# Kernel tuning notes

Hardware: AMD Instinct MI355X
Metric: run time of the kernel (lower is better)

The kernel has to match this reference:

```python
import jax, jax.numpy as jnp
import numpy as np

N, B, D_IN, HID = 1024, 8, 256, 256
L, SH, LH, GH = 2, 2, 4, 2
H = SH + LH + GH
DH = HID // H
EPS = 1e-5


def _sinusoidal_pe(n, d):
    pos = np.arange(n, dtype=np.float32)[:, None]
    i = np.arange(d, dtype=np.float32)[None, :]
    angle = pos / np.power(10000.0, (2.0 * np.floor(i / 2.0)) / d)
    pe = np.where((np.arange(d) % 2) == 0, np.sin(angle), np.cos(angle))
    return jnp.asarray(pe, jnp.float32)  # (n, d)


def _ln(x, g, b):
    mu = x.mean(-1, keepdims=True)
    var = ((x - mu) ** 2).mean(-1, keepdims=True)
    return (x - mu) * jax.lax.rsqrt(var + EPS) * g + b


def setup_inputs() -> dict:
    key = jax.random.key(0)
    ks = jax.random.split(key, 16)
    s = 0.02
    inp = {
        "nodes": jax.random.normal(ks[0], (N, B, D_IN), jnp.float32),
        "dist": jax.random.randint(ks[1], (B, N, N), 0, 6, jnp.int32),
        "W_in": jax.random.normal(ks[2], (D_IN, HID), jnp.float32) * s,
        "b_in": jnp.zeros((HID,), jnp.float32),
        "ln_in_g": jnp.ones((HID,), jnp.float32),
        "ln_in_b": jnp.zeros((HID,), jnp.float32),
        "Wqkv": jax.random.normal(ks[3], (L, HID, 3 * HID), jnp.float32) * s,
        "bqkv": jnp.zeros((L, 3 * HID), jnp.float32),
        "Wo": jax.random.normal(ks[4], (L, HID, HID), jnp.float32) * s,
        "bo": jnp.zeros((L, HID), jnp.float32),
        "ln1_g": jnp.ones((L, HID), jnp.float32),
        "ln1_b": jnp.zeros((L, HID), jnp.float32),
        "W1": jax.random.normal(ks[5], (L, HID, 2 * HID), jnp.float32) * s,
        "b1": jnp.zeros((L, 2 * HID), jnp.float32),
        "W2": jax.random.normal(ks[6], (L, 2 * HID, HID), jnp.float32) * s,
        "b2": jnp.zeros((L, HID), jnp.float32),
        "ln2_g": jnp.ones((L, HID), jnp.float32),
        "ln2_b": jnp.zeros((L, HID), jnp.float32),
        "bn_g": jnp.ones((HID,), jnp.float32),
        "bn_b": jnp.zeros((HID,), jnp.float32),
    }
    return inp


def reference(nodes, dist, W_in, b_in, ln_in_g, ln_in_b, Wqkv, bqkv, Wo, bo,
              ln1_g, ln1_b, W1, b1, W2, b2, ln2_g, ln2_b, bn_g, bn_b):
    # positional embedding (sinusoidal, added) + dense + LayerNorm; dropout=eval (identity)
    x = nodes + _sinusoidal_pe(N, D_IN)[:, None, :]          # (N,B,D_IN)
    x = _ln(x @ W_in + b_in, ln_in_g, ln_in_b)               # (N,B,HID)

    # dist_to_mask: per-head-group allowed patterns; True in torch mask = disallowed
    short = (dist == 1)[:, None]                             # (B,1,N,N)
    longm = (dist >= 1)[:, None]
    allowed = jnp.concatenate([
        jnp.broadcast_to(short, (B, SH, N, N)),
        jnp.broadcast_to(longm, (B, LH, N, N)),
        jnp.ones((B, GH, N, N), bool),
    ], axis=1)                                               # (B,H,N,N)
    bias = jnp.where(allowed, 0.0, -jnp.inf).astype(x.dtype)

    scale = 1.0 / np.sqrt(DH)
    for l in range(L):
        qkv = x @ Wqkv[l] + bqkv[l]                          # (N,B,3*HID)
        q, k, v = jnp.split(qkv, 3, axis=-1)
        def heads(t):  # (N,B,HID) -> (B,H,N,DH)
            return t.reshape(N, B, H, DH).transpose(1, 2, 0, 3)
        q, k, v = heads(q), heads(k), heads(v)
        s = jnp.einsum('bhnd,bhmd->bhnm', q, k) * scale + bias
        a = jax.nn.softmax(s, axis=-1)
        o = jnp.einsum('bhnm,bhmd->bhnd', a, v)              # (B,H,N,DH)
        o = o.transpose(2, 0, 1, 3).reshape(N, B, HID)
        x = _ln(x + o @ Wo[l] + bo[l], ln1_g[l], ln1_b[l])   # post-norm
        f = jax.nn.relu(x @ W1[l] + b1[l]) @ W2[l] + b2[l]
        x = _ln(x + f, ln2_g[l], ln2_b[l])

    y = x[0]                                                 # (B,HID) first position
    mu = y.mean(0)
    var = ((y - mu) ** 2).mean(0)
    return (y - mu) * jax.lax.rsqrt(var + EPS) * bn_g + bn_b
```

## Files before the change

### kernel.cpp

```cpp
#include <hip/hip_runtime.h>
#include <math.h>

constexpr int Nn = 1024, Bb = 8, HIDc = 256, Hh = 8, DHc = 32;

typedef __bf16 bf16x8 __attribute__((ext_vector_type(8)));
typedef __bf16 bf16x4 __attribute__((ext_vector_type(4)));
typedef float  f32x4  __attribute__((ext_vector_type(4)));

struct WCvtArgs {
    const float* src[9];
    int K[9], M[9], dstOff[9], tiles[9];
};

__global__ __launch_bounds__(256)
void prep_k(WCvtArgs a, __bf16* __restrict__ Wt,
            const int* __restrict__ dist, unsigned char* __restrict__ mp,
            const float* __restrict__ nodes, __bf16* __restrict__ xinb)
{
    __shared__ float ts[32][33];
    const int tid = threadIdx.x;
    if (blockIdx.x < 1088) {
        int bid = blockIdx.x, i = 0;
        while (bid >= a.tiles[i]) { bid -= a.tiles[i]; ++i; }
        const int K = a.K[i], M = a.M[i];
        const int tilesM = M >> 5;
        const int m0 = (bid % tilesM) << 5, k0 = (bid / tilesM) << 5;
        const float* src = a.src[i];
        __bf16* dst = Wt + a.dstOff[i];
        const int tx = tid & 31, ty = tid >> 5;
        #pragma unroll
        for (int j = 0; j < 4; ++j)
            ts[ty + 8 * j][tx] = src[(size_t)(k0 + ty + 8 * j) * M + m0 + tx];
        __syncthreads();
        #pragma unroll
        for (int j = 0; j < 4; ++j)
            dst[(size_t)(m0 + ty + 8 * j) * K + k0 + tx] = (__bf16)ts[tx][ty + 8 * j];
    } else if (blockIdx.x < 3136) {
        const int idx = (blockIdx.x - 1088) * 256 + tid;
        const int quad = idx & 3, c = (idx >> 2) & 15, q = (idx >> 6) & 1023, b = idx >> 16;
        const int* dp = dist + ((((size_t)b << 10) + q) << 10) + c * 64 + quad * 4;
        uchar4 out;
        unsigned char* po = &out.x;
        #pragma unroll
        for (int t = 0; t < 4; ++t) {
            const int4 v = *(const int4*)(dp + t * 16);
            unsigned int code = 0;
            const int dd[4] = {v.x, v.y, v.z, v.w};
            #pragma unroll
            for (int r = 0; r < 4; ++r)
                code |= ((dd[r] == 1 ? 1u : 0u) | (dd[r] >= 1 ? 2u : 0u)) << (2 * r);
            po[t] = (unsigned char)code;
        }
        *(uchar4*)(mp + ((((size_t)b << 10) + q) << 8) + (c << 4) + (quad << 2)) = out;
    } else {
        const int idx = (blockIdx.x - 3136) * 256 + tid;
        const int token = idx >> 7, k2 = (idx & 127) * 2;
        const int b = token >> 10, n = token & 1023;
        const float e = (float)k2 * (1.0f / 256.0f);
        const float freq = exp2f(-13.287712379549449f * e);
        const float ang = (float)n * freq;
        const float2 nd = *(const float2*)(nodes + ((size_t)(n * 8 + b)) * 256 + k2);
        __bf16* p = xinb + (size_t)token * 256 + k2;
        p[0] = (__bf16)(nd.x + sinf(ang));
        p[1] = (__bf16)(nd.y + cosf(ang));
    }
}

template<int NCH>
__device__ __forceinline__ void gemm8(const bf16x8* af, const __bf16* __restrict__ wsrc,
                                      __bf16 (*wlds)[72], int mrow, int kcol,
                                      int ch, int col, int quad, f32x4* acc)
{
    constexpr int K = NCH * 64;
    bf16x8 wreg[8];
    #pragma unroll
    for (int i = 0; i < 8; ++i)
        wreg[i] = *(const bf16x8*)(wsrc + (size_t)(i * 32 + mrow) * K + kcol);
    #pragma unroll
    for (int t = 0; t < 8; ++t) acc[t] = (f32x4){0.f, 0.f, 0.f, 0.f};
    for (int ck = 0; ck < NCH; ++ck) {
        __syncthreads();
        #pragma unroll
        for (int i = 0; i < 8; ++i)
            *(bf16x8*)&wlds[i * 32 + mrow][kcol] = wreg[i];
        if (ck + 1 < NCH) {
            #pragma unroll
            for (int i = 0; i < 8; ++i)
                wreg[i] = *(const bf16x8*)(wsrc + (size_t)(i * 32 + mrow) * K + (ck + 1) * 64 + kcol);
        }
        __syncthreads();
        #pragma unroll
        for (int t = 0; t < 8; ++t)
            #pragma unroll
            for (int kc = 0; kc < 2; ++kc) {
                const bf16x8 bfr = *(const bf16x8*)(&wlds[ch * 128 + t * 16 + col][kc * 32 + quad * 8]);
                acc[t] = __builtin_amdgcn_mfma_f32_16x16x32_bf16(af[ck * 2 + kc], bfr, acc[t], 0, 0, 0);
            }
    }
}

template<bool RESID, bool FFN, bool QKV, bool LASTX>
__global__ __launch_bounds__(256)
void layer_k(const __bf16* __restrict__ Ain, const float* __restrict__ xres,
             const __bf16* __restrict__ w0, const float* __restrict__ b0,
             const float* __restrict__ g1, const float* __restrict__ be1,
             const __bf16* __restrict__ w1, const float* __restrict__ b1_,
             const __bf16* __restrict__ w2, const float* __restrict__ b2_,
             const float* __restrict__ g2, const float* __restrict__ be2,
             const __bf16* __restrict__ wq, const float* __restrict__ bq,
             float* __restrict__ xout,
             __bf16* __restrict__ qb, __bf16* __restrict__ kb, __bf16* __restrict__ vtb)
{
    __shared__ char smem[36864];
    __bf16 (*wlds)[72]  = (__bf16 (*)[72])smem;
    __bf16 (*trans)[520] = (__bf16 (*)[520])smem;
    __shared__ float red[2][2][16][2];

    const int tid = threadIdx.x;
    const int lane = tid & 63;
    const int wv = tid >> 6;
    const int rt = wv >> 1, ch = wv & 1;
    const int col = lane & 15, quad = lane >> 4;
    const int row0 = blockIdx.x * 32;
    const int rowL = rt * 16 + col;
    const int mrow = tid >> 3, kcol = (tid & 7) * 8;
    const int trow = rt * 16 + quad * 4;

    bf16x8 afA[8];
    #pragma unroll
    for (int kc = 0; kc < 8; ++kc)
        afA[kc] = *(const bf16x8*)(Ain + (size_t)(row0 + rowL) * 256 + kc * 32 + quad * 8);
    f32x4 acc[8];
    gemm8<4>(afA, w0, wlds, mrow, kcol, ch, col, quad, acc);

    float val[4][8];
    {
        float bb[8], gm[8], bt[8];
        #pragma unroll
        for (int t = 0; t < 8; ++t) {
            const int cc = ch * 128 + t * 16 + col;
            bb[t] = b0[cc]; gm[t] = g1[cc]; bt[t] = be1[cc];
        }
        #pragma unroll
        for (int r = 0; r < 4; ++r) {
            float s1 = 0.f, s2 = 0.f;
            #pragma unroll
            for (int t = 0; t < 8; ++t) {
                float v = acc[t][r] + bb[t];
                if (RESID) v += xres[(size_t)(row0 + trow + r) * 256 + ch * 128 + t * 16 + col];
                val[r][t] = v; s1 += v; s2 += v * v;
            }
            s1 += __shfl_xor(s1, 1); s1 += __shfl_xor(s1, 2);
            s1 += __shfl_xor(s1, 4); s1 += __shfl_xor(s1, 8);
            s2 += __shfl_xor(s2, 1); s2 += __shfl_xor(s2, 2);
            s2 += __shfl_xor(s2, 4); s2 += __shfl_xor(s2, 8);
            if (col == 0) { red[rt][ch][quad * 4 + r][0] = s1; red[rt][ch][quad * 4 + r][1] = s2; }
        }
        __syncthreads();
        #pragma unroll
        for (int r = 0; r < 4; ++r) {
            const int qr = quad * 4 + r;
            const float s1 = red[rt][0][qr][0] + red[rt][1][qr][0];
            const float s2 = red[rt][0][qr][1] + red[rt][1][qr][1];
            const float mu = s1 * (1.0f / 256.0f);
            const float rv = rsqrtf(s2 * (1.0f / 256.0f) - mu * mu + 1e-5f);
            #pragma unroll
            for (int t = 0; t < 8; ++t) {
                const float o = (val[r][t] - mu) * rv * gm[t] + bt[t];
                val[r][t] = o;
                trans[trow + r][ch * 128 + t * 16 + col] = (__bf16)o;
                if (!FFN)
                    xout[(size_t)(row0 + trow + r) * 256 + ch * 128 + t * 16 + col] = o;
            }
        }
        __syncthreads();
    }

    if (FFN) {
        bf16x8 af1[8];
        #pragma unroll
        for (int kc = 0; kc < 8; ++kc)
            af1[kc] = *(const bf16x8*)(&trans[rowL][kc * 32 + quad * 8]);
        bf16x4 h1p[2][8];
        #pragma unroll
        for (int mh = 0; mh < 2; ++mh) {
            f32x4 accb[8];
            gemm8<4>(af1, w1 + (size_t)mh * 256 * 256, wlds, mrow, kcol, ch, col, quad, accb);
            #pragma unroll
            for (int t = 0; t < 8; ++t) {
                const float bbv = b1_[mh * 256 + ch * 128 + t * 16 + col];
                #pragma unroll
                for (int r = 0; r < 4; ++r)
                    h1p[mh][t][r] = (__bf16)fmaxf(accb[t][r] + bbv, 0.f);
            }
        }
        __syncthreads();
        #pragma unroll
        for (int mh = 0; mh < 2; ++mh)
            #pragma unroll
            for (int t = 0; t < 8; ++t)
                #pragma unroll
                for (int r = 0; r < 4; ++r)
                    trans[trow + r][mh * 256 + ch * 128 + t * 16 + col] = h1p[mh][t][r];
        __syncthreads();

        bf16x8 af2[16];
        #pragma unroll
        for (int kc = 0; kc < 16; ++kc)
            af2[kc] = *(const bf16x8*)(&trans[rowL][kc * 32 + quad * 8]);
        f32x4 accc[8];
        gemm8<8>(af2, w2, wlds, mrow, kcol, ch, col, quad, accc);

        float bb[8], gm[8], bt[8];
        #pragma unroll
        for (int t = 0; t < 8; ++t) {
            const int cc = ch * 128 + t * 16 + col;
            bb[t] = b2_[cc]; gm[t] = g2[cc]; bt[t] = be2[cc];
        }
        #pragma unroll
        for (int r = 0; r < 4; ++r) {
            float s1 = 0.f, s2 = 0.f;
            #pragma unroll
            for (int t = 0; t < 8; ++t) {
                const float v = accc[t][r] + bb[t] + val[r][t];
                val[r][t] = v; s1 += v; s2 += v * v;
            }
            s1 += __shfl_xor(s1, 1); s1 += __shfl_xor(s1, 2);
            s1 += __shfl_xor(s1, 4); s1 += __shfl_xor(s1, 8);
            s2 += __shfl_xor(s2, 1); s2 += __shfl_xor(s2, 2);
            s2 += __shfl_xor(s2, 4); s2 += __shfl_xor(s2, 8);
            if (col == 0) { red[rt][ch][quad * 4 + r][0] = s1; red[rt][ch][quad * 4 + r][1] = s2; }
        }
        __syncthreads();
        #pragma unroll
        for (int r = 0; r < 4; ++r) {
            const int qr = quad * 4 + r;
            const float s1 = red[rt][0][qr][0] + red[rt][1][qr][0];
            const float s2 = red[rt][0][qr][1] + red[rt][1][qr][1];
            const float mu = s1 * (1.0f / 256.0f);
            const float rv = rsqrtf(s2 * (1.0f / 256.0f) - mu * mu + 1e-5f);
            const int row = row0 + trow + r;
            #pragma unroll
            for (int t = 0; t < 8; ++t) {
                const float o = (val[r][t] - mu) * rv * gm[t] + bt[t];
                if (QKV) trans[trow + r][ch * 128 + t * 16 + col] = (__bf16)o;
                if (!LASTX)
                    xout[(size_t)row * 256 + ch * 128 + t * 16 + col] = o;
                else if ((row & 1023) == 0)
                    xout[(size_t)row * 256 + ch * 128 + t * 16 + col] = o;
            }
        }
        __syncthreads();
    }

    if (QKV) {
        bf16x8 af3[8];
        #pragma unroll
        for (int kc = 0; kc < 8; ++kc)
            af3[kc] = *(const bf16x8*)(&trans[rowL][kc * 32 + quad * 8]);
        const int bq_ = row0 >> 10;
        const int n0q = (row0 & 1023) + trow;
        for (int cg = 0; cg < 3; ++cg) {
            f32x4 accq[8];
            gemm8<4>(af3, wq + (size_t)cg * 256 * 256, wlds, mrow, kcol, ch, col, quad, accq);
            if (cg == 2) {
                #pragma unroll
                for (int t = 0; t < 8; ++t) {
                    const int cc = ch * 128 + t * 16 + col;
                    const int h = cc >> 5, dh = cc & 31;
                    const float bbv = bq[512 + cc];
                    bf16x4 p;
                    #pragma unroll
                    for (int r = 0; r < 4; ++r) p[r] = (__bf16)(accq[t][r] + bbv);
                    *(bf16x4*)(vtb + ((((size_t)(bq_ * 8 + h)) * 32 + dh) << 10) + n0q) = p;
                }
            } else {
                const float qs = (cg == 0) ? 0.25505402616305625f : 1.0f;
                __bf16* dst = (cg == 0) ? qb : kb;
                #pragma unroll
                for (int t = 0; t < 8; ++t) {
                    const int cc = ch * 128 + t * 16 + col;
                    const int h = cc >> 5, dh = cc & 31;
                    const float bbv = bq[cg * 256 + cc];
                    #pragma unroll
                    for (int r = 0; r < 4; ++r)
                        dst[((((size_t)(bq_ * 8 + h)) << 10) + n0q + r) * 32 + dh] =
                            (__bf16)((accq[t][r] + bbv) * qs);
                }
            }
        }
    }
}

__global__ __launch_bounds__(256)
void attn_mfma(const __bf16* __restrict__ Qb, const __bf16* __restrict__ Kb,
               const __bf16* __restrict__ Vt, const unsigned char* __restrict__ MP,
               __bf16* __restrict__ O)
{
    __shared__ __bf16 pbuf[2][4][2][16][72];
    const int tid = threadIdx.x;
    const int lane = tid & 63;
    const int wv = tid >> 6;
    const int col = lane & 15;
    const int quad = lane >> 4;
    const int xr = blockIdx.x;
    const int bh = ((xr & 7) << 3) | (xr >> 3);
    const int b = bh >> 3, h = bh & 7;
    const int qbase = blockIdx.y * 128 + wv * 32;
    const int hsel = (h < 2) ? 0 : 1;
    const bool masked = (h < 6);

    bf16x8 qf[2];
    #pragma unroll
    for (int j = 0; j < 2; ++j)
        qf[j] = *(const bf16x8*)(Qb + ((size_t)bh * Nn + qbase + j * 16 + col) * DHc + quad * 8);

    bf16x8 onesf;
    {
        const __bf16 one = (__bf16)1.0f, zero = (__bf16)0.0f;
        #pragma unroll
        for (int j = 0; j < 8; ++j) onesf[j] = (col == 0) ? one : zero;
    }

    f32x4 O0[2], O1[2], OL[2];
    #pragma unroll
    for (int j = 0; j < 2; ++j) {
        O0[j] = (f32x4){0.f, 0.f, 0.f, 0.f};
        O1[j] = (f32x4){0.f, 0.f, 0.f, 0.f};
        OL[j] = (f32x4){0.f, 0.f, 0.f, 0.f};
    }
    const f32x4 zf = {0.f, 0.f, 0.f, 0.f};
    const __bf16* kbase = Kb + (size_t)bh * Nn * DHc;

    bf16x8 kf[4];
    #pragma unroll
    for (int t = 0; t < 4; ++t)
        kf[t] = *(const bf16x8*)(kbase + (size_t)(t * 16 + col) * DHc + quad * 8);

    for (int c = 0; c < 16; ++c) {
        bf16x8 kn[4];
        if (c < 15)
            #pragma unroll
            for (int t = 0; t < 4; ++t)
                kn[t] = *(const bf16x8*)(kbase + (size_t)((c + 1) * 64 + t * 16 + col) * DHc + quad * 8);
        uchar4 mk[2];
        if (masked)
            #pragma unroll
            for (int j = 0; j < 2; ++j)
                mk[j] = *(const uchar4*)(MP + ((((size_t)b << 10) + qbase + j * 16 + col) << 8)
                                            + (c << 4) + (quad << 2));
        #pragma unroll
        for (int j = 0; j < 2; ++j) {
            f32x4 S[4];
            #pragma unroll
            for (int t = 0; t < 4; ++t)
                S[t] = __builtin_amdgcn_mfma_f32_16x16x32_bf16(kf[t], qf[j], zf, 0, 0, 0);
            if (masked) {
                const unsigned char mb[4] = {mk[j].x, mk[j].y, mk[j].z, mk[j].w};
                #pragma unroll
                for (int t = 0; t < 4; ++t)
                    #pragma unroll
                    for (int r = 0; r < 4; ++r)
                        if (!((mb[t] >> (2 * r + hsel)) & 1)) S[t][r] = -INFINITY;
            }
            #pragma unroll
            for (int t = 0; t < 4; ++t) {
                bf16x4 p4;
                #pragma unroll
                for (int r = 0; r < 4; ++r)
                    p4[r] = (__bf16)__builtin_amdgcn_exp2f(S[t][r]);
                *(bf16x4*)(&pbuf[c & 1][wv][j][col][t * 16 + quad * 4]) = p4;
            }
        }
        const __bf16* vp = Vt + (size_t)bh * DHc * Nn + c * 64 + quad * 8;
        #pragma unroll
        for (int kh = 0; kh < 2; ++kh) {
            const bf16x8 v0 = *(const bf16x8*)(vp + (size_t)col * Nn + kh * 32);
            const bf16x8 v1 = *(const bf16x8*)(vp + (size_t)(col + 16) * Nn + kh * 32);
            #pragma unroll
            for (int j = 0; j < 2; ++j) {
                const bf16x8 pf = *(const bf16x8*)(&pbuf[c & 1][wv][j][col][kh * 32 + quad * 8]);
                O0[j] = __builtin_amdgcn_mfma_f32_16x16x32_bf16(pf, v0, O0[j], 0, 0, 0);
                O1[j] = __builtin_amdgcn_mfma_f32_16x16x32_bf16(pf, v1, O1[j], 0, 0, 0);
                OL[j] = __builtin_amdgcn_mfma_f32_16x16x32_bf16(pf, onesf, OL[j], 0, 0, 0);
            }
        }
        if (c < 15)
            #pragma unroll
            for (int t = 0; t < 4; ++t) kf[t] = kn[t];
    }
    #pragma unroll
    for (int j = 0; j < 2; ++j)
        #pragma unroll
        for (int r = 0; r < 4; ++r) {
            const float Lr = __shfl(OL[j][r], lane & 48);
            const float inv = 1.0f / Lr;
            const int q = qbase + j * 16 + quad * 4 + r;
            __bf16* op = O + ((size_t)(b * 1024 + q)) * 256 + h * 32 + col;
            op[0]  = (__bf16)(O0[j][r] * inv);
            op[16] = (__bf16)(O1[j][r] * inv);
        }
}

__global__ __launch_bounds__(256)
void final_bn(const float* __restrict__ x, const float* __restrict__ g,
              const float* __restrict__ bta, float* __restrict__ out)
{
    const int d = threadIdx.x;
    float y[8]; float mu = 0.0f;
    #pragma unroll
    for (int i = 0; i < 8; ++i) { y[i] = x[((size_t)i << 18) + d]; mu += y[i]; }
    mu *= 0.125f;
    float var = 0.0f;
    #pragma unroll
    for (int i = 0; i < 8; ++i) { const float dd = y[i] - mu; var += dd * dd; }
    var *= 0.125f;
    const float r = rsqrtf(var + 1e-5f);
    const float gg = g[d], bb = bta[d];
    #pragma unroll
    for (int i = 0; i < 8; ++i) out[i * 256 + d] = (y[i] - mu) * r * gg + bb;
}

extern "C" void kernel_launch(void* const* d_in, const int* in_sizes, int n_in,
                              void* d_out, int out_size, void* d_ws, size_t ws_size,
                              hipStream_t stream)
{
    const float* nodes   = (const float*)d_in[0];
    const int*   dist    = (const int*)  d_in[1];
    const float* W_in    = (const float*)d_in[2];
    const float* b_in    = (const float*)d_in[3];
    const float* ln_in_g = (const float*)d_in[4];
    const float* ln_in_b = (const float*)d_in[5];
    const float* Wqkv    = (const float*)d_in[6];
    const float* bqkv    = (const float*)d_in[7];
    const float* Wo      = (const float*)d_in[8];
    const float* bo      = (const float*)d_in[9];
    const float* ln1_g   = (const float*)d_in[10];
    const float* ln1_b   = (const float*)d_in[11];
    const float* W1      = (const float*)d_in[12];
    const float* b1      = (const float*)d_in[13];
    const float* W2      = (const float*)d_in[14];
    const float* b2      = (const float*)d_in[15];
    const float* ln2_g   = (const float*)d_in[16];
    const float* ln2_b   = (const float*)d_in[17];
    const float* bn_g    = (const float*)d_in[18];
    const float* bn_b    = (const float*)d_in[19];

    char* ws = (char*)d_ws;
    float*  x   = (float*)(ws);
    unsigned char* mp = (unsigned char*)(ws + 8388608);
    __bf16* wt  = (__bf16*)(ws + 10485760);
    __bf16* qb  = (__bf16*)(ws + 12845056);
    __bf16* kb  = (__bf16*)(ws + 17039360);
    __bf16* vtb = (__bf16*)(ws + 21233664);
    __bf16* ob  = (__bf16*)(ws + 25427968);
    __bf16* xinb = ob;

    WCvtArgs wa;
    wa.src[0] = W_in;           wa.K[0] = 256; wa.M[0] = 256; wa.dstOff[0] = 0;
    wa.src[1] = Wqkv;           wa.K[1] = 256; wa.M[1] = 768; wa.dstOff[1] = 65536;
    wa.src[2] = Wqkv + 196608;  wa.K[2] = 256; wa.M[2] = 768; wa.dstOff[2] = 262144;
    wa.src[3] = Wo;             wa.K[3] = 256; wa.M[3] = 256; wa.dstOff[3] = 458752;
    wa.src[4] = Wo + 65536;     wa.K[4] = 256; wa.M[4] = 256; wa.dstOff[4] = 524288;
    wa.src[5] = W1;             wa.K[5] = 256; wa.M[5] = 512; wa.dstOff[5] = 589824;
    wa.src[6] = W1 + 131072;    wa.K[6] = 256; wa.M[6] = 512; wa.dstOff[6] = 720896;
    wa.src[7] = W2;             wa.K[7] = 512; wa.M[7] = 256; wa.dstOff[7] = 851968;
    wa.src[8] = W2 + 131072;    wa.K[8] = 512; wa.M[8] = 256; wa.dstOff[8] = 983040;
    for (int i = 0; i < 9; ++i) wa.tiles[i] = (wa.K[i] >> 5) * (wa.M[i] >> 5);

    prep_k<<<7232, 256, 0, stream>>>(wa, wt, dist, mp, nodes, xinb);

    layer_k<false, false, true, false><<<256, 256, 0, stream>>>(
        xinb, nullptr, wt, b_in, ln_in_g, ln_in_b,
        nullptr, nullptr, nullptr, nullptr, nullptr, nullptr,
        wt + 65536, bqkv, x, qb, kb, vtb);

    attn_mfma<<<dim3(64, 8), 256, 0, stream>>>(qb, kb, vtb, mp, ob);

    layer_k<true, true, true, false><<<256, 256, 0, stream>>>(
        ob, x, wt + 458752, bo, ln1_g, ln1_b,
        wt + 589824, b1, wt + 851968, b2, ln2_g, ln2_b,
        wt + 262144, bqkv + 768, x, qb, kb, vtb);

    attn_mfma<<<dim3(64, 8), 256, 0, stream>>>(qb, kb, vtb, mp, ob);

    layer_k<true, true, false, true><<<256, 256, 0, stream>>>(
        ob, x, wt + 524288, bo + 256, ln1_g + 256, ln1_b + 256,
        wt + 720896, b1 + 512, wt + 983040, b2 + 256, ln2_g + 256, ln2_b + 256,
        nullptr, nullptr, x, nullptr, nullptr, nullptr);

    final_bn<<<1, 256, 0, stream>>>(x, bn_g, bn_b, (float*)d_out);
}
```

Before: 263.0 us.

## Prune last layer to position-0 rows and double-buffer weight tiles in LDS

Only position 0 of each batch feeds the final output, so the last layer now computes Q only for blocks holding position 0, runs attention for a single query tile (grid 64x1) and runs the final layer kernel as one block on the 8 position-0 rows. K and V are still computed for every token. The GEMM weight staging in LDS is also double-buffered so the next chunk's store overlaps the current MFMAs, with one barrier per chunk instead of two. This doubles the shared memory per block, which may reduce occupancy. It also relies on the attention grid's first tile covering query row 0 for all batches.

```diff
diff --git a/kernel.cpp b/kernel.cpp
--- a/kernel.cpp
+++ b/kernel.cpp
@@ -68,7 +68,7 @@
 
 template<int NCH>
 __device__ __forceinline__ void gemm8(const bf16x8* af, const __bf16* __restrict__ wsrc,
-                                      __bf16 (*wlds)[72], int mrow, int kcol,
+                                      __bf16 (*wlds)[256][72], int mrow, int kcol,
                                       int ch, int col, int quad, f32x4* acc)
 {
     constexpr int K = NCH * 64;
@@ -76,30 +76,41 @@
     #pragma unroll
     for (int i = 0; i < 8; ++i)
         wreg[i] = *(const bf16x8*)(wsrc + (size_t)(i * 32 + mrow) * K + kcol);
+    __syncthreads();
+    #pragma unroll
+    for (int i = 0; i < 8; ++i)
+        *(bf16x8*)&wlds[0][i * 32 + mrow][kcol] = wreg[i];
+    if (NCH > 1) {
+        #pragma unroll
+        for (int i = 0; i < 8; ++i)
+            wreg[i] = *(const bf16x8*)(wsrc + (size_t)(i * 32 + mrow) * K + 64 + kcol);
+    }
+    __syncthreads();
     #pragma unroll
     for (int t = 0; t < 8; ++t) acc[t] = (f32x4){0.f, 0.f, 0.f, 0.f};
     for (int ck = 0; ck < NCH; ++ck) {
-        __syncthreads();
-        #pragma unroll
-        for (int i = 0; i < 8; ++i)
-            *(bf16x8*)&wlds[i * 32 + mrow][kcol] = wreg[i];
+        #pragma unroll
+        for (int t = 0; t < 8; ++t)
+            #pragma unroll
+            for (int kc = 0; kc < 2; ++kc) {
+                const bf16x8 bfr = *(const bf16x8*)(&wlds[ck & 1][ch * 128 + t * 16 + col][kc * 32 + quad * 8]);
+                acc[t] = __builtin_amdgcn_mfma_f32_16x16x32_bf16(af[ck * 2 + kc], bfr, acc[t], 0, 0, 0);
+            }
         if (ck + 1 < NCH) {
             #pragma unroll
             for (int i = 0; i < 8; ++i)
-                wreg[i] = *(const bf16x8*)(wsrc + (size_t)(i * 32 + mrow) * K + (ck + 1) * 64 + kcol);
-        }
-        __syncthreads();
-        #pragma unroll
-        for (int t = 0; t < 8; ++t)
-            #pragma unroll
-            for (int kc = 0; kc < 2; ++kc) {
-                const bf16x8 bfr = *(const bf16x8*)(&wlds[ch * 128 + t * 16 + col][kc * 32 + quad * 8]);
-                acc[t] = __builtin_amdgcn_mfma_f32_16x16x32_bf16(af[ck * 2 + kc], bfr, acc[t], 0, 0, 0);
-            }
+                *(bf16x8*)&wlds[(ck + 1) & 1][i * 32 + mrow][kcol] = wreg[i];
+            if (ck + 2 < NCH) {
+                #pragma unroll
+                for (int i = 0; i < 8; ++i)
+                    wreg[i] = *(const bf16x8*)(wsrc + (size_t)(i * 32 + mrow) * K + (ck + 2) * 64 + kcol);
+            }
+        }
+        __syncthreads();
     }
 }
 
-template<bool RESID, bool FFN, bool QKV, bool LASTX>
+template<bool RESID, bool FFN, bool QKV, bool N0ROWS, bool XGATE>
 __global__ __launch_bounds__(256)
 void layer_k(const __bf16* __restrict__ Ain, const float* __restrict__ xres,
              const __bf16* __restrict__ w0, const float* __restrict__ b0,
@@ -107,12 +118,12 @@
              const __bf16* __restrict__ w1, const float* __restrict__ b1_,
              const __bf16* __restrict__ w2, const float* __restrict__ b2_,
              const float* __restrict__ g2, const float* __restrict__ be2,
-             const __bf16* __restrict__ wq, const float* __restrict__ bq,
+             const __bf16* __restrict__ wq, const float* __restrict__ bq, int qfull,
              float* __restrict__ xout,
              __bf16* __restrict__ qb, __bf16* __restrict__ kb, __bf16* __restrict__ vtb)
 {
-    __shared__ char smem[36864];
-    __bf16 (*wlds)[72]  = (__bf16 (*)[72])smem;
+    __shared__ char smem[73728];
+    __bf16 (*wlds)[256][72] = (__bf16 (*)[256][72])smem;
     __bf16 (*trans)[520] = (__bf16 (*)[520])smem;
     __shared__ float red[2][2][16][2];
 
@@ -126,10 +137,12 @@
     const int mrow = tid >> 3, kcol = (tid & 7) * 8;
     const int trow = rt * 16 + quad * 4;
 
+    const int rowAg = N0ROWS ? ((rowL & 7) << 10) : (row0 + rowL);
+
     bf16x8 afA[8];
     #pragma unroll
     for (int kc = 0; kc < 8; ++kc)
-        afA[kc] = *(const bf16x8*)(Ain + (size_t)(row0 + rowL) * 256 + kc * 32 + quad * 8);
+        afA[kc] = *(const bf16x8*)(Ain + (size_t)rowAg * 256 + kc * 32 + quad * 8);
     f32x4 acc[8];
     gemm8<4>(afA, w0, wlds, mrow, kcol, ch, col, quad, acc);
 
@@ -143,11 +156,12 @@
         }
         #pragma unroll
         for (int r = 0; r < 4; ++r) {
+            const int rg = N0ROWS ? (((trow + r) & 7) << 10) : (row0 + trow + r);
             float s1 = 0.f, s2 = 0.f;
             #pragma unroll
             for (int t = 0; t < 8; ++t) {
                 float v = acc[t][r] + bb[t];
-                if (RESID) v += xres[(size_t)(row0 + trow + r) * 256 + ch * 128 + t * 16 + col];
+                if (RESID) v += xres[(size_t)rg * 256 + ch * 128 + t * 16 + col];
                 val[r][t] = v; s1 += v; s2 += v * v;
             }
             s1 += __shfl_xor(s1, 1); s1 += __shfl_xor(s1, 2);
@@ -239,15 +253,17 @@
             const float s2 = red[rt][0][qr][1] + red[rt][1][qr][1];
             const float mu = s1 * (1.0f / 256.0f);
             const float rv = rsqrtf(s2 * (1.0f / 256.0f) - mu * mu + 1e-5f);
-            const int row = row0 + trow + r;
+            const int rl = trow + r;
+            const int rg = N0ROWS ? ((rl & 7) << 10) : (row0 + rl);
             #pragma unroll
             for (int t = 0; t < 8; ++t) {
                 const float o = (val[r][t] - mu) * rv * gm[t] + bt[t];
-                if (QKV) trans[trow + r][ch * 128 + t * 16 + col] = (__bf16)o;
-                if (!LASTX)
-                    xout[(size_t)row * 256 + ch * 128 + t * 16 + col] = o;
-                else if ((row & 1023) == 0)
-                    xout[(size_t)row * 256 + ch * 128 + t * 16 + col] = o;
+                if (QKV) trans[rl][ch * 128 + t * 16 + col] = (__bf16)o;
+                bool wr;
+                if (N0ROWS)      wr = (rl < 8);
+                else if (XGATE)  wr = ((rg & 1023) == 0);
+                else             wr = true;
+                if (wr) xout[(size_t)rg * 256 + ch * 128 + t * 16 + col] = o;
             }
         }
         __syncthreads();
@@ -260,7 +276,9 @@
             af3[kc] = *(const bf16x8*)(&trans[rowL][kc * 32 + quad * 8]);
         const int bq_ = row0 >> 10;
         const int n0q = (row0 & 1023) + trow;
+        const bool qneed = qfull || ((row0 & 1023) == 0);
         for (int cg = 0; cg < 3; ++cg) {
+            if (cg == 0 && !qneed) continue;
             f32x4 accq[8];
             gemm8<4>(af3, wq + (size_t)cg * 256 * 256, wlds, mrow, kcol, ch, col, quad, accq);
             if (cg == 2) {
@@ -470,24 +488,24 @@
 
     prep_k<<<7232, 256, 0, stream>>>(wa, wt, dist, mp, nodes, xinb);
 
-    layer_k<false, false, true, false><<<256, 256, 0, stream>>>(
+    layer_k<false, false, true, false, false><<<256, 256, 0, stream>>>(
         xinb, nullptr, wt, b_in, ln_in_g, ln_in_b,
         nullptr, nullptr, nullptr, nullptr, nullptr, nullptr,
-        wt + 65536, bqkv, x, qb, kb, vtb);
+        wt + 65536, bqkv, 1, x, qb, kb, vtb);
 
     attn_mfma<<<dim3(64, 8), 256, 0, stream>>>(qb, kb, vtb, mp, ob);
 
-    layer_k<true, true, true, false><<<256, 256, 0, stream>>>(
+    layer_k<true, true, true, false, true><<<256, 256, 0, stream>>>(
         ob, x, wt + 458752, bo, ln1_g, ln1_b,
         wt + 589824, b1, wt + 851968, b2, ln2_g, ln2_b,
-        wt + 262144, bqkv + 768, x, qb, kb, vtb);
-
-    attn_mfma<<<dim3(64, 8), 256, 0, stream>>>(qb, kb, vtb, mp, ob);
-
-    layer_k<true, true, false, true><<<256, 256, 0, stream>>>(
+        wt + 262144, bqkv + 768, 0, x, qb, kb, vtb);
+
+    attn_mfma<<<dim3(64, 1), 256, 0, stream>>>(qb, kb, vtb, mp, ob);
+
+    layer_k<true, true, false, true, true><<<1, 256, 0, stream>>>(
         ob, x, wt + 524288, bo + 256, ln1_g + 256, ln1_b + 256,
         wt + 720896, b1 + 512, wt + 983040, b2 + 256, ln2_g + 256, ln2_b + 256,
-        nullptr, nullptr, x, nullptr, nullptr, nullptr);
+        nullptr, nullptr, 0, x, nullptr, nullptr, nullptr);
 
     final_bn<<<1, 256, 0, stream>>>(x, bn_g, bn_b, (float*)d_out);
 }
```

After: 252.7 us. -3.9%, faster.
